# Optimization experiments

Hardware: AMD Instinct MI355X
Metric: run time of the kernel (lower is better)

The kernel has to match this reference:

```python
import jax, jax.numpy as jnp
import numpy as np

N = 100000
IN_F, HID, OUT = 256, 128, 64
NNZ = 1600000
EQ = 200000


def setup_inputs() -> dict:
    key = jax.random.key(0)
    ks = jax.random.split(key, 10)
    x = jax.random.normal(ks[0], (N, IN_F), dtype=jnp.float32)
    adj_rows = jnp.sort(jax.random.randint(ks[1], (NNZ,), 0, N, dtype=jnp.int32))
    adj_cols = jax.random.randint(ks[2], (NNZ,), 0, N, dtype=jnp.int32)
    adj_vals = jax.random.uniform(ks[3], (NNZ,), dtype=jnp.float32)
    edge_index = jax.random.randint(ks[4], (2, EQ), 0, N, dtype=jnp.int32)
    # params (torch Linear default init: U(-1/sqrt(fan_in), 1/sqrt(fan_in)))
    s1 = 1.0 / np.sqrt(IN_F)
    W1 = jax.random.uniform(ks[5], (IN_F, HID), minval=-s1, maxval=s1, dtype=jnp.float32)
    b1 = jax.random.uniform(ks[6], (HID,), minval=-s1, maxval=s1, dtype=jnp.float32)
    s2 = 1.0 / np.sqrt(HID)
    W2 = jax.random.uniform(ks[7], (HID, OUT), minval=-s2, maxval=s2, dtype=jnp.float32)
    b2 = jax.random.uniform(ks[8], (OUT,), minval=-s2, maxval=s2, dtype=jnp.float32)
    return {"x": x, "adj_rows": adj_rows, "adj_cols": adj_cols, "adj_vals": adj_vals,
            "edge_index": edge_index, "W1": W1, "b1": b1, "W2": W2, "b2": b2}


def spmm(rows, cols, vals, dense):
    # out[i,:] = sum_{e: rows[e]==i} vals[e] * dense[cols[e],:]
    msgs = vals[:, None] * dense[cols]  # [nnz, d]
    return jax.ops.segment_sum(msgs, rows, num_segments=N)


def reference(x, adj_rows, adj_cols, adj_vals, edge_index, W1, b1, W2, b2):
    # GCN layer 1: linear then sparse aggregation
    h = spmm(adj_rows, adj_cols, adj_vals, x @ W1 + b1)  # [N, HID]
    h = jax.nn.relu(h)  # dropout is identity in eval mode
    # GCN layer 2
    z = spmm(adj_rows, adj_cols, adj_vals, h @ W2 + b2)  # [N, OUT]
    # decode: gather src/dst embeddings, elementwise dot
    src, dst = edge_index[0], edge_index[1]
    return jnp.sum(z[src] * z[dst], axis=1)  # [EQ]
```

## Files before the change

### kernel.cpp

```cpp
#include <hip/hip_runtime.h>

constexpr int NN    = 100000;
constexpr int NNZ_E = 1600000;
constexpr int EQn   = 200000;
constexpr int INF_  = 256;
constexpr int HIDF  = 128;
constexpr int OUTF  = 64;

typedef float  f32x4  __attribute__((ext_vector_type(4)));
typedef short  bf16x8 __attribute__((ext_vector_type(8)));

__device__ inline unsigned short f2bf(float f) {
    union { float f; unsigned int i; } x; x.f = f;
    unsigned int r = x.i + 0x7fffu + ((x.i >> 16) & 1u);
    return (unsigned short)(r >> 16);
}

__device__ inline void gl2lds16(const void* g, void* l) {
    __builtin_amdgcn_global_load_lds(
        (const __attribute__((address_space(1))) void*)g,
        (__attribute__((address_space(3))) void*)l, 16, 0, 0);
}

__global__ __launch_bounds__(256) void build_row_ptr(const int* __restrict__ rows,
                                                     int* __restrict__ ptr) {
    int i = blockIdx.x * 256 + threadIdx.x;
    if (i > NN) return;
    int lo = 0, hi = NNZ_E;
    while (lo < hi) {
        int mid = (lo + hi) >> 1;
        if (rows[mid] < i) lo = mid + 1; else hi = mid;
    }
    ptr[i] = lo;
}

__global__ __launch_bounds__(256) void convert_weights(const float* __restrict__ W1,
                                                       const float* __restrict__ W2,
                                                       unsigned short* __restrict__ W1t,
                                                       unsigned short* __restrict__ W2t) {
    int i = blockIdx.x * 256 + threadIdx.x;
    if (i < INF_ * HIDF) {
        int k = i >> 7, n = i & 127;
        W1t[n * INF_ + k] = f2bf(W1[i]);
    }
    if (i < HIDF * OUTF) {
        int k = i >> 6, n = i & 63;
        W2t[n * HIDF + k] = f2bf(W2[i]);
    }
}

template<int K, int NCOLS, int TR, int CGB, bool A_IS_BF16>
__global__ __launch_bounds__(512, 1) void gemm_persist(const void* __restrict__ Av,
                                                       const unsigned short* __restrict__ Bt,
                                                       const float* __restrict__ bias,
                                                       unsigned short* __restrict__ C,
                                                       int M) {
    constexpr int KS   = K / 32;
    constexpr int NT   = 2;
    constexpr int CG   = 1 << CGB;
    constexpr int RB   = 8 / CG;
    static_assert(RB * 16 == TR, "tile rows = 16*RB");
    static_assert(CG * 32 == NCOLS, "cols = 32*CG");
    constexpr int ABPR = A_IS_BF16 ? K * 2 : K * 4;
    constexpr int RPC  = 1024 / ABPR;
    constexpr int NCH  = TR / RPC;
    constexpr int CPWW = NCH / 8;
    constexpr int ABUF = NCH * 1040;
    constexpr int PK   = K + 8;
    constexpr int PADW = NCOLS + 8;
    constexpr int BSB  = NCOLS * PK * 2;
    constexpr int EPB  = TR * PADW * 2;
    static_assert(TR * NCOLS / 8 == 512, "one uint4 store per thread");
    __shared__ __align__(16) unsigned char smem[2 * ABUF + BSB + EPB];
    unsigned char*  Ab = smem;
    unsigned short* Bs = (unsigned short*)(smem + 2 * ABUF);
    unsigned short* ep = (unsigned short*)(smem + 2 * ABUF + BSB);

    const int tid  = threadIdx.x;
    const int wave = tid >> 6;
    const int lane = tid & 63;
    const int quad = lane >> 4;
    const int l16  = lane & 15;
    const int cg   = wave & (CG - 1);
    const int rb   = wave >> CGB;

    for (int i = tid; i < NCOLS * K / 8; i += 512) {
        int n = i / (K / 8), kc = (i % (K / 8)) * 8;
        *(uint4*)&Bs[n * PK + kc] = *(const uint4*)&Bt[(size_t)n * K + kc];
    }

    const int ntiles = (M + TR - 1) / TR;
    const char* abase = (const char*)Av;

    auto stage = [&](int b, int tile0) {
        unsigned char* dst = Ab + b * ABUF;
        #pragma unroll
        for (int j = 0; j < CPWW; ++j) {
            int ch = wave * CPWW + j;
            int r0 = tile0 + ch * RPC;
            if (r0 > M - RPC) r0 = M - RPC;
            gl2lds16(abase + (size_t)r0 * ABPR + lane * 16, dst + ch * 1040);
        }
    };

    int t = blockIdx.x, buf = 0;
    if (t < ntiles) stage(0, t * TR);

    for (; t < ntiles; t += gridDim.x) {
        __syncthreads();
        int tn = t + gridDim.x;
        if (tn < ntiles) stage(1 - buf, tn * TR);

        const unsigned char* ab = Ab + buf * ABUF;
        const int arow = rb * 16 + l16;
        f32x4 acc[NT];
        #pragma unroll
        for (int tt = 0; tt < NT; ++tt) acc[tt] = (f32x4){0.f, 0.f, 0.f, 0.f};

        #pragma unroll
        for (int ks = 0; ks < KS; ++ks) {
            bf16x8 af;
            if constexpr (A_IS_BF16) {
                int flat = arow * ABPR + ks * 64 + quad * 16;
                af = *(const bf16x8*)(ab + (flat >> 10) * 1040 + (flat & 1023));
            } else {
                int flat = arow * ABPR + ks * 128 + quad * 32;
                const unsigned char* p = ab + (flat >> 10) * 1040 + (flat & 1023);
                float4 a0 = *(const float4*)p;
                float4 a1 = *(const float4*)(p + 16);
                af[0] = (short)f2bf(a0.x); af[1] = (short)f2bf(a0.y);
                af[2] = (short)f2bf(a0.z); af[3] = (short)f2bf(a0.w);
                af[4] = (short)f2bf(a1.x); af[5] = (short)f2bf(a1.y);
                af[6] = (short)f2bf(a1.z); af[7] = (short)f2bf(a1.w);
            }
            #pragma unroll
            for (int tt = 0; tt < NT; ++tt) {
                bf16x8 bfr = *(const bf16x8*)&Bs[(cg * 32 + tt * 16 + l16) * PK + ks * 32 + quad * 8];
                acc[tt] = __builtin_amdgcn_mfma_f32_16x16x32_bf16(af, bfr, acc[tt], 0, 0, 0);
            }
        }

        #pragma unroll
        for (int tt = 0; tt < NT; ++tt) {
            const int col = cg * 32 + tt * 16 + l16;
            const float bb = bias[col];
            #pragma unroll
            for (int r = 0; r < 4; ++r)
                ep[(rb * 16 + quad * 4 + r) * PADW + col] = f2bf(acc[tt][r] + bb);
        }
        __syncthreads();
        {
            constexpr int CH = NCOLS / 8;
            int r = tid / CH, cc = tid % CH;
            int grow = t * TR + r;
            if (grow < M)
                *(uint4*)&C[(size_t)grow * NCOLS + cc * 8] =
                    *(const uint4*)&ep[r * PADW + cc * 8];
        }
        buf ^= 1;
    }
}

__device__ inline void fma8_bf16(float* acc, uint4 q, float v) {
    union { unsigned int i; float f; } t;
    #pragma unroll
    for (int p = 0; p < 4; ++p) {
        unsigned int w = (&q.x)[p];
        t.i = w << 16;          acc[2*p]   += v * t.f;
        t.i = w & 0xffff0000u;  acc[2*p+1] += v * t.f;
    }
}

template<int D, bool RELU>
__global__ __launch_bounds__(256) void spmm_bf16(const int* __restrict__ ptr,
                                                 const int* __restrict__ cols,
                                                 const float* __restrict__ vals,
                                                 const unsigned short* __restrict__ dense,
                                                 unsigned short* __restrict__ outm) {
    constexpr int LPR = D / 8;
    constexpr int RPB = 256 / LPR;
    const int lane = threadIdx.x % LPR;
    const int row  = blockIdx.x * RPB + threadIdx.x / LPR;
    if (row >= NN) return;

    int e = ptr[row];
    const int e1 = ptr[row + 1];
    const size_t lo8 = (size_t)lane * 8;
    float acc[8] = {};

    for (; e + 4 <= e1; e += 4) {
        int   c0 = cols[e],   c1 = cols[e+1], c2 = cols[e+2], c3 = cols[e+3];
        float v0 = vals[e],   v1 = vals[e+1], v2 = vals[e+2], v3 = vals[e+3];
        uint4 q0 = *(const uint4*)&dense[(size_t)c0 * D + lo8];
        uint4 q1 = *(const uint4*)&dense[(size_t)c1 * D + lo8];
        uint4 q2 = *(const uint4*)&dense[(size_t)c2 * D + lo8];
        uint4 q3 = *(const uint4*)&dense[(size_t)c3 * D + lo8];
        fma8_bf16(acc, q0, v0);
        fma8_bf16(acc, q1, v1);
        fma8_bf16(acc, q2, v2);
        fma8_bf16(acc, q3, v3);
    }
    for (; e < e1; ++e) {
        int   c = cols[e];
        float v = vals[e];
        uint4 q = *(const uint4*)&dense[(size_t)c * D + lo8];
        fma8_bf16(acc, q, v);
    }

    if (RELU) {
        #pragma unroll
        for (int p = 0; p < 8; ++p) acc[p] = fmaxf(acc[p], 0.f);
    }
    uint4 o;
    #pragma unroll
    for (int p = 0; p < 4; ++p)
        (&o.x)[p] = (unsigned int)f2bf(acc[2*p]) | ((unsigned int)f2bf(acc[2*p+1]) << 16);
    *(uint4*)&outm[(size_t)row * D + lo8] = o;
}

__global__ __launch_bounds__(256) void decode_dot_bf16(const unsigned short* __restrict__ z,
                                                       const int* __restrict__ ei,
                                                       float* __restrict__ outv) {
    const int lane = threadIdx.x & 7;
    const int e    = blockIdx.x * 32 + (threadIdx.x >> 3);
    if (e >= EQn) return;
    const int s = ei[e];
    const int d = ei[EQn + e];
    uint4 qa = *(const uint4*)&z[(size_t)s * 64 + lane * 8];
    uint4 qb = *(const uint4*)&z[(size_t)d * 64 + lane * 8];
    union { unsigned int i; float f; } ta, tb;
    float p = 0.f;
    #pragma unroll
    for (int k = 0; k < 4; ++k) {
        unsigned int wa = (&qa.x)[k], wb = (&qb.x)[k];
        ta.i = wa << 16;         tb.i = wb << 16;         p += ta.f * tb.f;
        ta.i = wa & 0xffff0000u; tb.i = wb & 0xffff0000u; p += ta.f * tb.f;
    }
    p += __shfl_xor(p, 1, 8);
    p += __shfl_xor(p, 2, 8);
    p += __shfl_xor(p, 4, 8);
    if (lane == 0) outv[e] = p;
}

extern "C" void kernel_launch(void* const* d_in, const int* in_sizes, int n_in,
                              void* d_out, int out_size, void* d_ws, size_t ws_size,
                              hipStream_t stream) {
    (void)in_sizes; (void)n_in; (void)out_size; (void)ws_size;

    const float* x        = (const float*)d_in[0];
    const int*   adj_rows = (const int*)  d_in[1];
    const int*   adj_cols = (const int*)  d_in[2];
    const float* adj_vals = (const float*)d_in[3];
    const int*   ei       = (const int*)  d_in[4];
    const float* W1       = (const float*)d_in[5];
    const float* b1       = (const float*)d_in[6];
    const float* W2       = (const float*)d_in[7];
    const float* b2       = (const float*)d_in[8];
    float* out = (float*)d_out;

    char* ws = (char*)d_ws;
    int* row_ptr = (int*)ws;
    size_t off = ((size_t)(NN + 1) * sizeof(int) + 511) & ~(size_t)511;
    unsigned short* W1t = (unsigned short*)(ws + off);
    unsigned short* W2t = W1t + (size_t)HIDF * INF_;
    unsigned short* slotA = W2t + (size_t)OUTF * HIDF;
    slotA = (unsigned short*)(((size_t)slotA + 511) & ~(size_t)511);
    unsigned short* slotB = slotA + (size_t)NN * HIDF;

    build_row_ptr<<<(NN + 256) / 256, 256, 0, stream>>>(adj_rows, row_ptr);
    convert_weights<<<(INF_ * HIDF + 255) / 256, 256, 0, stream>>>(W1, W2, W1t, W2t);

    gemm_persist<INF_, HIDF, 32, 2, false><<<256, 512, 0, stream>>>(
        x, W1t, b1, slotA, NN);

    spmm_bf16<HIDF, true><<<(NN + 15) / 16, 256, 0, stream>>>(
        row_ptr, adj_cols, adj_vals, slotA, slotB);

    gemm_persist<HIDF, OUTF, 64, 1, true><<<512, 512, 0, stream>>>(
        slotB, W2t, b2, slotA, NN);

    spmm_bf16<OUTF, false><<<(NN + 31) / 32, 256, 0, stream>>>(
        row_ptr, adj_cols, adj_vals, slotA, slotB);

    decode_dot_bf16<<<EQn / 32, 256, 0, stream>>>(slotB, ei, out);
}
```

Measured before the change: 300.8 us.

## Merge prep kernels, batch SpMM tail loads, two edges per decode group

Fuses the row-pointer binary search and the weight conversion into one prep kernel, removing a launch. The SpMM remainder loop becomes one predicated batch of three gathers with clamped indices and zeroed weights, so the tail loads can be in flight together instead of one after another. The decode kernel handles two query edges per 8-lane group, which halves the grid and raises memory-level parallelism per thread. Each piece is small: the tail may issue redundant loads, and the decode change adds register pressure.

After: 292.6 us. -2.7%, faster.

```diff
diff --git a/kernel.cpp b/kernel.cpp
--- a/kernel.cpp
+++ b/kernel.cpp
@@ -22,23 +22,21 @@
         (__attribute__((address_space(3))) void*)l, 16, 0, 0);
 }
 
-__global__ __launch_bounds__(256) void build_row_ptr(const int* __restrict__ rows,
-                                                     int* __restrict__ ptr) {
+__global__ __launch_bounds__(256) void prep(const int* __restrict__ rows,
+                                            int* __restrict__ ptr,
+                                            const float* __restrict__ W1,
+                                            const float* __restrict__ W2,
+                                            unsigned short* __restrict__ W1t,
+                                            unsigned short* __restrict__ W2t) {
     int i = blockIdx.x * 256 + threadIdx.x;
-    if (i > NN) return;
-    int lo = 0, hi = NNZ_E;
-    while (lo < hi) {
-        int mid = (lo + hi) >> 1;
-        if (rows[mid] < i) lo = mid + 1; else hi = mid;
-    }
-    ptr[i] = lo;
-}
-
-__global__ __launch_bounds__(256) void convert_weights(const float* __restrict__ W1,
-                                                       const float* __restrict__ W2,
-                                                       unsigned short* __restrict__ W1t,
-                                                       unsigned short* __restrict__ W2t) {
-    int i = blockIdx.x * 256 + threadIdx.x;
+    if (i <= NN) {
+        int lo = 0, hi = NNZ_E;
+        while (lo < hi) {
+            int mid = (lo + hi) >> 1;
+            if (rows[mid] < i) lo = mid + 1; else hi = mid;
+        }
+        ptr[i] = lo;
+    }
     if (i < INF_ * HIDF) {
         int k = i >> 7, n = i & 127;
         W1t[n * INF_ + k] = f2bf(W1[i]);
@@ -188,23 +186,32 @@
     const size_t lo8 = (size_t)lane * 8;
     float acc[8] = {};
 
-    for (; e + 4 <= e1; e += 4) {
-        int   c0 = cols[e],   c1 = cols[e+1], c2 = cols[e+2], c3 = cols[e+3];
-        float v0 = vals[e],   v1 = vals[e+1], v2 = vals[e+2], v3 = vals[e+3];
-        uint4 q0 = *(const uint4*)&dense[(size_t)c0 * D + lo8];
-        uint4 q1 = *(const uint4*)&dense[(size_t)c1 * D + lo8];
-        uint4 q2 = *(const uint4*)&dense[(size_t)c2 * D + lo8];
-        uint4 q3 = *(const uint4*)&dense[(size_t)c3 * D + lo8];
-        fma8_bf16(acc, q0, v0);
-        fma8_bf16(acc, q1, v1);
-        fma8_bf16(acc, q2, v2);
-        fma8_bf16(acc, q3, v3);
-    }
-    for (; e < e1; ++e) {
-        int   c = cols[e];
-        float v = vals[e];
-        uint4 q = *(const uint4*)&dense[(size_t)c * D + lo8];
-        fma8_bf16(acc, q, v);
+    if (e < e1) {
+        for (; e + 4 <= e1; e += 4) {
+            int   c0 = cols[e],   c1 = cols[e+1], c2 = cols[e+2], c3 = cols[e+3];
+            float v0 = vals[e],   v1 = vals[e+1], v2 = vals[e+2], v3 = vals[e+3];
+            uint4 q0 = *(const uint4*)&dense[(size_t)c0 * D + lo8];
+            uint4 q1 = *(const uint4*)&dense[(size_t)c1 * D + lo8];
+            uint4 q2 = *(const uint4*)&dense[(size_t)c2 * D + lo8];
+            uint4 q3 = *(const uint4*)&dense[(size_t)c3 * D + lo8];
+            fma8_bf16(acc, q0, v0);
+            fma8_bf16(acc, q1, v1);
+            fma8_bf16(acc, q2, v2);
+            fma8_bf16(acc, q3, v3);
+        }
+        if (e < e1) {
+            int i1 = e, i2 = e + 1, i3 = e + 2;
+            bool k1 = i1 < e1, k2 = i2 < e1, k3 = i3 < e1;
+            i1 = k1 ? i1 : e1 - 1; i2 = k2 ? i2 : e1 - 1; i3 = k3 ? i3 : e1 - 1;
+            int   c0 = cols[i1],            c1 = cols[i2],            c2 = cols[i3];
+            float v0 = k1 ? vals[i1] : 0.f, v1 = k2 ? vals[i2] : 0.f, v2 = k3 ? vals[i3] : 0.f;
+            uint4 q0 = *(const uint4*)&dense[(size_t)c0 * D + lo8];
+            uint4 q1 = *(const uint4*)&dense[(size_t)c1 * D + lo8];
+            uint4 q2 = *(const uint4*)&dense[(size_t)c2 * D + lo8];
+            fma8_bf16(acc, q0, v0);
+            fma8_bf16(acc, q1, v1);
+            fma8_bf16(acc, q2, v2);
+        }
     }
 
     if (RELU) {
@@ -221,25 +228,32 @@
 __global__ __launch_bounds__(256) void decode_dot_bf16(const unsigned short* __restrict__ z,
                                                        const int* __restrict__ ei,
                                                        float* __restrict__ outv) {
+    constexpr int HALF = EQn / 2;
     const int lane = threadIdx.x & 7;
-    const int e    = blockIdx.x * 32 + (threadIdx.x >> 3);
-    if (e >= EQn) return;
-    const int s = ei[e];
-    const int d = ei[EQn + e];
-    uint4 qa = *(const uint4*)&z[(size_t)s * 64 + lane * 8];
-    uint4 qb = *(const uint4*)&z[(size_t)d * 64 + lane * 8];
+    const int g    = blockIdx.x * 32 + (threadIdx.x >> 3);
+    if (g >= HALF) return;
+    const int eA = g, eB = g + HALF;
+    const int sA = ei[eA],       dA = ei[EQn + eA];
+    const int sB = ei[eB],       dB = ei[EQn + eB];
+    uint4 qa0 = *(const uint4*)&z[(size_t)sA * 64 + lane * 8];
+    uint4 qb0 = *(const uint4*)&z[(size_t)dA * 64 + lane * 8];
+    uint4 qa1 = *(const uint4*)&z[(size_t)sB * 64 + lane * 8];
+    uint4 qb1 = *(const uint4*)&z[(size_t)dB * 64 + lane * 8];
     union { unsigned int i; float f; } ta, tb;
-    float p = 0.f;
+    float p0 = 0.f, p1 = 0.f;
     #pragma unroll
     for (int k = 0; k < 4; ++k) {
-        unsigned int wa = (&qa.x)[k], wb = (&qb.x)[k];
-        ta.i = wa << 16;         tb.i = wb << 16;         p += ta.f * tb.f;
-        ta.i = wa & 0xffff0000u; tb.i = wb & 0xffff0000u; p += ta.f * tb.f;
-    }
-    p += __shfl_xor(p, 1, 8);
-    p += __shfl_xor(p, 2, 8);
-    p += __shfl_xor(p, 4, 8);
-    if (lane == 0) outv[e] = p;
+        unsigned int wa = (&qa0.x)[k], wb = (&qb0.x)[k];
+        ta.i = wa << 16;         tb.i = wb << 16;         p0 += ta.f * tb.f;
+        ta.i = wa & 0xffff0000u; tb.i = wb & 0xffff0000u; p0 += ta.f * tb.f;
+        wa = (&qa1.x)[k]; wb = (&qb1.x)[k];
+        ta.i = wa << 16;         tb.i = wb << 16;         p1 += ta.f * tb.f;
+        ta.i = wa & 0xffff0000u; tb.i = wb & 0xffff0000u; p1 += ta.f * tb.f;
+    }
+    p0 += __shfl_xor(p0, 1, 8); p1 += __shfl_xor(p1, 1, 8);
+    p0 += __shfl_xor(p0, 2, 8); p1 += __shfl_xor(p1, 2, 8);
+    p0 += __shfl_xor(p0, 4, 8); p1 += __shfl_xor(p1, 4, 8);
+    if (lane == 0) { outv[eA] = p0; outv[eB] = p1; }
 }
 
 extern "C" void kernel_launch(void* const* d_in, const int* in_sizes, int n_in,
@@ -267,8 +281,7 @@
     slotA = (unsigned short*)(((size_t)slotA + 511) & ~(size_t)511);
     unsigned short* slotB = slotA + (size_t)NN * HIDF;
 
-    build_row_ptr<<<(NN + 256) / 256, 256, 0, stream>>>(adj_rows, row_ptr);
-    convert_weights<<<(INF_ * HIDF + 255) / 256, 256, 0, stream>>>(W1, W2, W1t, W2t);
+    prep<<<(NN + 256) / 256, 256, 0, stream>>>(adj_rows, row_ptr, W1, W2, W1t, W2t);
 
     gemm_persist<INF_, HIDF, 32, 2, false><<<256, 512, 0, stream>>>(
         x, W1t, b1, slotA, NN);
@@ -282,5 +295,5 @@
     spmm_bf16<OUTF, false><<<(NN + 31) / 32, 256, 0, stream>>>(
         row_ptr, adj_cols, adj_vals, slotA, slotB);
 
-    decode_dot_bf16<<<EQn / 32, 256, 0, stream>>>(slotB, ei, out);
-}
+    decode_dot_bf16<<<(EQn / 2) / 32, 256, 0, stream>>>(slotB, ei, out);
+}
```
